# Optimization experiments

Measured on AMD Instinct MI355X. Metric: run time of the kernel, lower is better.

Reference implementation:

```python
import jax, jax.numpy as jnp
import numpy as np

RADIUS = 0.05  # ball-query radius (original default 0.015 is too sparse for unit-cube density)


def setup_inputs() -> dict:
    key = jax.random.key(0)
    k1, k2, k3 = jax.random.split(key, 3)
    B, N_IN, N_OUT = 8, 16384, 8192
    x = jax.random.normal(k1, (B, N_IN), dtype=jnp.float32)
    inp_positions = jax.random.uniform(k2, (N_IN, 3), dtype=jnp.float32)
    out_positions = jax.random.uniform(k3, (N_OUT, 3), dtype=jnp.float32)
    return {"x": x, "inp_positions": inp_positions, "out_positions": out_positions}


def reference(x, inp_positions, out_positions):
    # Radius neighbor mean pooling: for each output point, average x over all
    # input points within RADIUS. Equivalent to the two spmm calls (sum and
    # count) followed by safe division in the original module.
    r2 = RADIUS * RADIUS
    # pairwise squared distances [n_out, n_in]
    d2 = jnp.sum((out_positions[:, None, :] - inp_positions[None, :, :]) ** 2, axis=-1)
    mask = (d2 <= r2).astype(x.dtype)          # sparse adjacency, dense-masked
    counts = jnp.sum(mask, axis=1)             # [n_out] = dem before clamping
    num = jnp.einsum("oi,bi->bo", mask, x)    # [B, n_out]
    dem = jnp.where(counts > 0, counts, jnp.ones_like(counts))
    return num / dem[None, :]
```

## Files before the change

### kernel.cpp

```cpp
#include <hip/hip_runtime.h>

#define TPB   256
#define BINT  64
#define MAXB  8
#define GD    20
#define NC    (GD * GD * GD)
#define CAP   16

static inline int cdiv(int a, int b) { return (a + b - 1) / b; }

#define DPP_ADD_I(x, ctrl, rmask)                                             \
    ((x) + __builtin_amdgcn_update_dpp(0, (x), (ctrl), (rmask), 0xf, true))
#define DPP_ADD_F(x, ctrl, rmask)                                             \
    ((x) + __int_as_float(__builtin_amdgcn_update_dpp(                        \
               0, __float_as_int(x), (ctrl), (rmask), 0xf, true)))

__device__ __forceinline__ int wave_incl_scan_i(int x) {
    x = DPP_ADD_I(x, 0x111, 0xf);
    x = DPP_ADD_I(x, 0x112, 0xf);
    x = DPP_ADD_I(x, 0x114, 0xf);
    x = DPP_ADD_I(x, 0x118, 0xf);
    x = DPP_ADD_I(x, 0x142, 0xa);
    x = DPP_ADD_I(x, 0x143, 0xc);
    return x;
}

template <int CTRL, int RMASK>
__device__ __forceinline__ int dpp_max_step(int x) {
    const int y = __builtin_amdgcn_update_dpp(0, x, CTRL, RMASK, 0xf, true);
    return ((unsigned)x > (unsigned)y) ? x : y;
}
__device__ __forceinline__ int wave_incl_maxscan_u(int x) {
    x = dpp_max_step<0x111, 0xf>(x);
    x = dpp_max_step<0x112, 0xf>(x);
    x = dpp_max_step<0x114, 0xf>(x);
    x = dpp_max_step<0x118, 0xf>(x);
    x = dpp_max_step<0x142, 0xa>(x);
    x = dpp_max_step<0x143, 0xc>(x);
    return x;
}

__device__ __forceinline__ float wave_sum_f(float x) {
    x = DPP_ADD_F(x, 0x111, 0xf);
    x = DPP_ADD_F(x, 0x112, 0xf);
    x = DPP_ADD_F(x, 0x114, 0xf);
    x = DPP_ADD_F(x, 0x118, 0xf);
    x = DPP_ADD_F(x, 0x142, 0xa);
    x = DPP_ADD_F(x, 0x143, 0xc);
    return __int_as_float(__builtin_amdgcn_readlane(__float_as_int(x), 63));
}

__global__ void __launch_bounds__(BINT) bin_kernel(
    const float* __restrict__ x, const float* __restrict__ ip,
    int* __restrict__ counts, float4* __restrict__ bins,
    float* __restrict__ xT, int B, int n_in)
{
    const int i = blockIdx.x * BINT + (int)threadIdx.x;
    if (i >= n_in) return;
    const float px = ip[3 * i], py = ip[3 * i + 1], pz = ip[3 * i + 2];
    const int cx = min(GD - 1, max(0, (int)(px * (float)GD)));
    const int cy = min(GD - 1, max(0, (int)(py * (float)GD)));
    const int cz = min(GD - 1, max(0, (int)(pz * (float)GD)));
    const int cell = (cx * GD + cy) * GD + cz;
    const int slot = atomicAdd(counts + cell, 1);
    if (slot < CAP)
        bins[(size_t)cell * CAP + slot] = make_float4(px, py, pz, __int_as_float(i));
    float v[MAXB];
#pragma unroll
    for (int b = 0; b < MAXB; ++b)
        v[b] = (b < B) ? x[(size_t)b * n_in + i] : 0.0f;
    float4* dst = (float4*)(xT + (size_t)i * MAXB);
    dst[0] = make_float4(v[0], v[1], v[2], v[3]);
    dst[1] = make_float4(v[4], v[5], v[6], v[7]);
}

__global__ void __launch_bounds__(TPB) query_kernel(
    const int* __restrict__ counts, const float4* __restrict__ bins,
    const float* __restrict__ xT, const float* __restrict__ out_pos,
    float* __restrict__ out, int B, int n_out, float r2)
{
    __shared__ int Msh[TPB / 64][64];

    const int lane = (int)threadIdx.x & 63;
    const int wid  = (int)threadIdx.x >> 6;
    const int o    = blockIdx.x * 4 + wid;
    if (o >= n_out) return;

    volatile int* M = &Msh[wid][0];

    const float ox = out_pos[3 * o];
    const float oy = out_pos[3 * o + 1];
    const float oz = out_pos[3 * o + 2];

    const float m = 0.05f + 1e-4f;
    const int cxlo = max(0, (int)floorf((ox - m) * (float)GD));
    const int cxhi = min(GD - 1, (int)floorf((ox + m) * (float)GD));
    const int cylo = max(0, (int)floorf((oy - m) * (float)GD));
    const int cyhi = min(GD - 1, (int)floorf((oy + m) * (float)GD));
    const int czlo = max(0, (int)floorf((oz - m) * (float)GD));
    const int czhi = min(GD - 1, (int)floorf((oz + m) * (float)GD));
    const int nx = cxhi - cxlo + 1, ny = cyhi - cylo + 1, nz = czhi - czlo + 1;
    const int ncell = nx * ny * nz;

    int cnt = 0, cellid = 0;
    if (lane < ncell) {
        int t = lane;
        const int dz = t % nz; t /= nz;
        const int dy = t % ny; t /= ny;
        const int dx = t;
        cellid = ((cxlo + dx) * GD + (cylo + dy)) * GD + (czlo + dz);
        cnt = min(counts[cellid], CAP);
    }

    const int incl = wave_incl_scan_i(cnt);
    const int T    = __builtin_amdgcn_readlane(incl, 63);
    const int excl = incl - cnt;
    const int pack = (excl << 13) | cellid;
    const bool pusher = (lane < ncell) && (cnt > 0);

    float csum = 0.0f;
    float acc[MAXB];
#pragma unroll
    for (int b = 0; b < MAXB; ++b) acc[b] = 0.0f;

    int seed = 0;
    for (int base = 0; base < T; base += 64) {
        const int t = base + lane;
        const bool act = t < T;

        M[lane] = 0;
        __builtin_amdgcn_wave_barrier();
        if (pusher && (unsigned)(excl - base) < 64u)
            M[excl - base] = pack;
        __builtin_amdgcn_wave_barrier();
        int r = M[lane];
        if (lane == 0) r = ((unsigned)r > (unsigned)seed) ? r : seed;
        const int own = wave_incl_maxscan_u(r);
        seed = __builtin_amdgcn_readlane(own, 63);

        const int ej = (unsigned)own >> 13;
        const int cj = own & 0x1FFF;
        float4 cand = make_float4(1e9f, 1e9f, 1e9f, 0.0f);
        if (act) cand = bins[(size_t)cj * CAP + (t - ej)];
        const float dx = ox - cand.x;
        const float dy = oy - cand.y;
        const float dz = oz - cand.z;
        const float d2 = dx * dx + dy * dy + dz * dz;
        if (d2 <= r2) {
            csum += 1.0f;
            const int idx = __float_as_int(cand.w);
            const float4* xv = (const float4*)(xT + (size_t)idx * MAXB);
            const float4 a = xv[0], b4 = xv[1];
            acc[0] += a.x;  acc[1] += a.y;  acc[2] += a.z;  acc[3] += a.w;
            acc[4] += b4.x; acc[5] += b4.y; acc[6] += b4.z; acc[7] += b4.w;
        }
    }

    const float tc = wave_sum_f(csum);
    const float t0 = wave_sum_f(acc[0]);
    const float t1 = wave_sum_f(acc[1]);
    const float t2 = wave_sum_f(acc[2]);
    const float t3 = wave_sum_f(acc[3]);
    const float t4 = wave_sum_f(acc[4]);
    const float t5 = wave_sum_f(acc[5]);
    const float t6 = wave_sum_f(acc[6]);
    const float t7 = wave_sum_f(acc[7]);

    const float cc = (tc > 0.0f) ? tc : 1.0f;
    float v = t0;
    v = (lane == 1) ? t1 : v;
    v = (lane == 2) ? t2 : v;
    v = (lane == 3) ? t3 : v;
    v = (lane == 4) ? t4 : v;
    v = (lane == 5) ? t5 : v;
    v = (lane == 6) ? t6 : v;
    v = (lane == 7) ? t7 : v;
    if (lane < B) out[(size_t)lane * n_out + o] = v / cc;
}

__global__ void __launch_bounds__(TPB) brute_kernel(
    const float* __restrict__ x, const float* __restrict__ ip,
    const float* __restrict__ op, float* __restrict__ out,
    int B, int n_in, int n_out, float r2)
{
    const int o = blockIdx.x * TPB + (int)threadIdx.x;
    if (o >= n_out) return;
    const float ox = op[3 * o], oy = op[3 * o + 1], oz = op[3 * o + 2];
    float cnt = 0.0f, acc[MAXB];
#pragma unroll
    for (int b = 0; b < MAXB; ++b) acc[b] = 0.0f;
    for (int i = 0; i < n_in; ++i) {
        const float dx = ox - ip[3 * i];
        const float dy = oy - ip[3 * i + 1];
        const float dz = oz - ip[3 * i + 2];
        const float d2 = dx * dx + dy * dy + dz * dz;
        if (d2 <= r2) {
            cnt += 1.0f;
            for (int b = 0; b < B && b < MAXB; ++b) acc[b] += x[(size_t)b * n_in + i];
        }
    }
    const float cc = (cnt > 0.0f) ? cnt : 1.0f;
    for (int b = 0; b < B && b < MAXB; ++b)
        out[(size_t)b * n_out + o] = acc[b] / cc;
}

extern "C" void kernel_launch(void* const* d_in, const int* in_sizes, int n_in_args,
                              void* d_out, int out_size, void* d_ws, size_t ws_size,
                              hipStream_t stream) {
    const float* x  = (const float*)d_in[0];
    const float* ip = (const float*)d_in[1];
    const float* op = (const float*)d_in[2];
    float* out = (float*)d_out;

    const int n_in  = in_sizes[1] / 3;
    const int n_out = in_sizes[2] / 3;
    const int B     = in_sizes[0] / n_in;
    const float r2  = (float)(0.05 * 0.05);

    const size_t counts_b = (size_t)NC * sizeof(int);
    const size_t bins_b   = (size_t)NC * CAP * sizeof(float4);
    const size_t xT_b     = (size_t)n_in * MAXB * sizeof(float);
    const size_t need     = counts_b + bins_b + xT_b;

    if (B <= MAXB && ws_size >= need) {
        int*    counts = (int*)d_ws;
        float4* bins   = (float4*)((char*)d_ws + counts_b);
        float*  xT     = (float*)((char*)d_ws + counts_b + bins_b);

        (void)hipMemsetAsync(counts, 0, counts_b, stream);
        bin_kernel<<<cdiv(n_in, BINT), BINT, 0, stream>>>(x, ip, counts, bins, xT,
                                                          B, n_in);
        query_kernel<<<cdiv(n_out, 4), TPB, 0, stream>>>(counts, bins, xT, op, out,
                                                         B, n_out, r2);
    } else {
        brute_kernel<<<cdiv(n_out, TPB), TPB, 0, stream>>>(x, ip, op, out,
                                                           B, n_in, n_out, r2);
    }
}
```

Baseline: 66.79 us.

## Fuse binning and query into one persistent kernel with a grid barrier

Merges the binning kernel and the query kernel into a single persistent launch of 1024 blocks. An atomic-counter grid barrier separates the binning phase from the query phase, and output points are processed in a grid-stride loop over waves. This removes a kernel launch and its inter-kernel gap. In exchange, the kernel depends on all blocks being co-resident, and the spin loop's bail-out could let a block proceed before binning finishes.

```diff
diff --git a/kernel.cpp b/kernel.cpp
--- a/kernel.cpp
+++ b/kernel.cpp
@@ -1,7 +1,7 @@
 #include <hip/hip_runtime.h>
 
 #define TPB   256
-#define BINT  64
+#define GRID  1024
 #define MAXB  8
 #define GD    20
 #define NC    (GD * GD * GD)
@@ -50,132 +50,148 @@
     return __int_as_float(__builtin_amdgcn_readlane(__float_as_int(x), 63));
 }
 
-__global__ void __launch_bounds__(BINT) bin_kernel(
+__global__ void __launch_bounds__(TPB, 4) fused_kernel(
     const float* __restrict__ x, const float* __restrict__ ip,
-    int* __restrict__ counts, float4* __restrict__ bins,
-    float* __restrict__ xT, int B, int n_in)
-{
-    const int i = blockIdx.x * BINT + (int)threadIdx.x;
-    if (i >= n_in) return;
-    const float px = ip[3 * i], py = ip[3 * i + 1], pz = ip[3 * i + 2];
-    const int cx = min(GD - 1, max(0, (int)(px * (float)GD)));
-    const int cy = min(GD - 1, max(0, (int)(py * (float)GD)));
-    const int cz = min(GD - 1, max(0, (int)(pz * (float)GD)));
-    const int cell = (cx * GD + cy) * GD + cz;
-    const int slot = atomicAdd(counts + cell, 1);
-    if (slot < CAP)
-        bins[(size_t)cell * CAP + slot] = make_float4(px, py, pz, __int_as_float(i));
-    float v[MAXB];
-#pragma unroll
-    for (int b = 0; b < MAXB; ++b)
-        v[b] = (b < B) ? x[(size_t)b * n_in + i] : 0.0f;
-    float4* dst = (float4*)(xT + (size_t)i * MAXB);
-    dst[0] = make_float4(v[0], v[1], v[2], v[3]);
-    dst[1] = make_float4(v[4], v[5], v[6], v[7]);
-}
-
-__global__ void __launch_bounds__(TPB) query_kernel(
-    const int* __restrict__ counts, const float4* __restrict__ bins,
-    const float* __restrict__ xT, const float* __restrict__ out_pos,
-    float* __restrict__ out, int B, int n_out, float r2)
+    const float* __restrict__ op,
+    int* __restrict__ counts, int* __restrict__ bar,
+    float4* __restrict__ bins, float* __restrict__ xT,
+    float* __restrict__ out, int B, int n_in, int n_out, float r2)
 {
     __shared__ int Msh[TPB / 64][64];
 
+    const int tid = (int)(blockIdx.x * TPB + threadIdx.x);
+
+    if (tid < n_in) {
+        const int i = tid;
+        const float px = ip[3 * i], py = ip[3 * i + 1], pz = ip[3 * i + 2];
+        const int cx = min(GD - 1, max(0, (int)(px * (float)GD)));
+        const int cy = min(GD - 1, max(0, (int)(py * (float)GD)));
+        const int cz = min(GD - 1, max(0, (int)(pz * (float)GD)));
+        const int cell = (cx * GD + cy) * GD + cz;
+        const int slot = atomicAdd(counts + cell, 1);
+        if (slot < CAP)
+            bins[(size_t)cell * CAP + slot] =
+                make_float4(px, py, pz, __int_as_float(i));
+        float v[MAXB];
+#pragma unroll
+        for (int b = 0; b < MAXB; ++b)
+            v[b] = (b < B) ? x[(size_t)b * n_in + i] : 0.0f;
+        float4* dst = (float4*)(xT + (size_t)i * MAXB);
+        dst[0] = make_float4(v[0], v[1], v[2], v[3]);
+        dst[1] = make_float4(v[4], v[5], v[6], v[7]);
+    }
+
+    __threadfence();
+    __syncthreads();
+    if (threadIdx.x == 0) {
+        atomicAdd(bar, 1);
+        int spins = 0;
+        while (__hip_atomic_load(bar, __ATOMIC_RELAXED,
+                                 __HIP_MEMORY_SCOPE_AGENT) < GRID) {
+            __builtin_amdgcn_s_sleep(8);
+            if (++spins > (1 << 20)) break;
+        }
+    }
+    __syncthreads();
+    __threadfence();
+
     const int lane = (int)threadIdx.x & 63;
     const int wid  = (int)threadIdx.x >> 6;
-    const int o    = blockIdx.x * 4 + wid;
-    if (o >= n_out) return;
-
+    const int wv   = tid >> 6;
+    const int nwv  = (GRID * TPB) >> 6;
     volatile int* M = &Msh[wid][0];
 
-    const float ox = out_pos[3 * o];
-    const float oy = out_pos[3 * o + 1];
-    const float oz = out_pos[3 * o + 2];
-
-    const float m = 0.05f + 1e-4f;
-    const int cxlo = max(0, (int)floorf((ox - m) * (float)GD));
-    const int cxhi = min(GD - 1, (int)floorf((ox + m) * (float)GD));
-    const int cylo = max(0, (int)floorf((oy - m) * (float)GD));
-    const int cyhi = min(GD - 1, (int)floorf((oy + m) * (float)GD));
-    const int czlo = max(0, (int)floorf((oz - m) * (float)GD));
-    const int czhi = min(GD - 1, (int)floorf((oz + m) * (float)GD));
-    const int nx = cxhi - cxlo + 1, ny = cyhi - cylo + 1, nz = czhi - czlo + 1;
-    const int ncell = nx * ny * nz;
-
-    int cnt = 0, cellid = 0;
-    if (lane < ncell) {
-        int t = lane;
-        const int dz = t % nz; t /= nz;
-        const int dy = t % ny; t /= ny;
-        const int dx = t;
-        cellid = ((cxlo + dx) * GD + (cylo + dy)) * GD + (czlo + dz);
-        cnt = min(counts[cellid], CAP);
-    }
-
-    const int incl = wave_incl_scan_i(cnt);
-    const int T    = __builtin_amdgcn_readlane(incl, 63);
-    const int excl = incl - cnt;
-    const int pack = (excl << 13) | cellid;
-    const bool pusher = (lane < ncell) && (cnt > 0);
-
-    float csum = 0.0f;
-    float acc[MAXB];
+    for (int o = wv; o < n_out; o += nwv) {
+        const float ox = op[3 * o];
+        const float oy = op[3 * o + 1];
+        const float oz = op[3 * o + 2];
+
+        const float m = 0.05f + 1e-4f;
+        const int cxlo = max(0, (int)floorf((ox - m) * (float)GD));
+        const int cxhi = min(GD - 1, (int)floorf((ox + m) * (float)GD));
+        const int cylo = max(0, (int)floorf((oy - m) * (float)GD));
+        const int cyhi = min(GD - 1, (int)floorf((oy + m) * (float)GD));
+        const int czlo = max(0, (int)floorf((oz - m) * (float)GD));
+        const int czhi = min(GD - 1, (int)floorf((oz + m) * (float)GD));
+        const int nx = cxhi - cxlo + 1, ny = cylo <= cyhi ? cyhi - cylo + 1 : 0,
+                  nz = czhi - czlo + 1;
+        const int ncell = nx * ny * nz;
+
+        int cnt = 0, cellid = 0;
+        if (lane < ncell) {
+            int t = lane;
+            const int dz = t % nz; t /= nz;
+            const int dy = t % ny; t /= ny;
+            const int dx = t;
+            cellid = ((cxlo + dx) * GD + (cylo + dy)) * GD + (czlo + dz);
+            cnt = min(counts[cellid], CAP);
+        }
+
+        const int incl = wave_incl_scan_i(cnt);
+        const int T    = __builtin_amdgcn_readlane(incl, 63);
+        const int excl = incl - cnt;
+        const int pack = (excl << 13) | cellid;
+        const bool pusher = (lane < ncell) && (cnt > 0);
+
+        float csum = 0.0f;
+        float acc[MAXB];
 #pragma unroll
-    for (int b = 0; b < MAXB; ++b) acc[b] = 0.0f;
-
-    int seed = 0;
-    for (int base = 0; base < T; base += 64) {
-        const int t = base + lane;
-        const bool act = t < T;
-
-        M[lane] = 0;
-        __builtin_amdgcn_wave_barrier();
-        if (pusher && (unsigned)(excl - base) < 64u)
-            M[excl - base] = pack;
-        __builtin_amdgcn_wave_barrier();
-        int r = M[lane];
-        if (lane == 0) r = ((unsigned)r > (unsigned)seed) ? r : seed;
-        const int own = wave_incl_maxscan_u(r);
-        seed = __builtin_amdgcn_readlane(own, 63);
-
-        const int ej = (unsigned)own >> 13;
-        const int cj = own & 0x1FFF;
-        float4 cand = make_float4(1e9f, 1e9f, 1e9f, 0.0f);
-        if (act) cand = bins[(size_t)cj * CAP + (t - ej)];
-        const float dx = ox - cand.x;
-        const float dy = oy - cand.y;
-        const float dz = oz - cand.z;
-        const float d2 = dx * dx + dy * dy + dz * dz;
-        if (d2 <= r2) {
-            csum += 1.0f;
-            const int idx = __float_as_int(cand.w);
-            const float4* xv = (const float4*)(xT + (size_t)idx * MAXB);
-            const float4 a = xv[0], b4 = xv[1];
-            acc[0] += a.x;  acc[1] += a.y;  acc[2] += a.z;  acc[3] += a.w;
-            acc[4] += b4.x; acc[5] += b4.y; acc[6] += b4.z; acc[7] += b4.w;
-        }
-    }
-
-    const float tc = wave_sum_f(csum);
-    const float t0 = wave_sum_f(acc[0]);
-    const float t1 = wave_sum_f(acc[1]);
-    const float t2 = wave_sum_f(acc[2]);
-    const float t3 = wave_sum_f(acc[3]);
-    const float t4 = wave_sum_f(acc[4]);
-    const float t5 = wave_sum_f(acc[5]);
-    const float t6 = wave_sum_f(acc[6]);
-    const float t7 = wave_sum_f(acc[7]);
-
-    const float cc = (tc > 0.0f) ? tc : 1.0f;
-    float v = t0;
-    v = (lane == 1) ? t1 : v;
-    v = (lane == 2) ? t2 : v;
-    v = (lane == 3) ? t3 : v;
-    v = (lane == 4) ? t4 : v;
-    v = (lane == 5) ? t5 : v;
-    v = (lane == 6) ? t6 : v;
-    v = (lane == 7) ? t7 : v;
-    if (lane < B) out[(size_t)lane * n_out + o] = v / cc;
+        for (int b = 0; b < MAXB; ++b) acc[b] = 0.0f;
+
+        int seed = 0;
+        for (int base = 0; base < T; base += 64) {
+            const int t = base + lane;
+            const bool act = t < T;
+
+            M[lane] = 0;
+            __builtin_amdgcn_wave_barrier();
+            if (pusher && (unsigned)(excl - base) < 64u)
+                M[excl - base] = pack;
+            __builtin_amdgcn_wave_barrier();
+            int r = M[lane];
+            if (lane == 0) r = ((unsigned)r > (unsigned)seed) ? r : seed;
+            const int own = wave_incl_maxscan_u(r);
+            seed = __builtin_amdgcn_readlane(own, 63);
+
+            const int ej = (unsigned)own >> 13;
+            const int cj = own & 0x1FFF;
+            float4 cand = make_float4(1e9f, 1e9f, 1e9f, 0.0f);
+            if (act) cand = bins[(size_t)cj * CAP + (t - ej)];
+            const float dx = ox - cand.x;
+            const float dy = oy - cand.y;
+            const float dz = oz - cand.z;
+            const float d2 = dx * dx + dy * dy + dz * dz;
+            if (d2 <= r2) {
+                csum += 1.0f;
+                const int idx = __float_as_int(cand.w);
+                const float4* xv = (const float4*)(xT + (size_t)idx * MAXB);
+                const float4 a = xv[0], b4 = xv[1];
+                acc[0] += a.x;  acc[1] += a.y;  acc[2] += a.z;  acc[3] += a.w;
+                acc[4] += b4.x; acc[5] += b4.y; acc[6] += b4.z; acc[7] += b4.w;
+            }
+        }
+
+        const float tc = wave_sum_f(csum);
+        const float t0 = wave_sum_f(acc[0]);
+        const float t1 = wave_sum_f(acc[1]);
+        const float t2 = wave_sum_f(acc[2]);
+        const float t3 = wave_sum_f(acc[3]);
+        const float t4 = wave_sum_f(acc[4]);
+        const float t5 = wave_sum_f(acc[5]);
+        const float t6 = wave_sum_f(acc[6]);
+        const float t7 = wave_sum_f(acc[7]);
+
+        const float cc = (tc > 0.0f) ? tc : 1.0f;
+        float v = t0;
+        v = (lane == 1) ? t1 : v;
+        v = (lane == 2) ? t2 : v;
+        v = (lane == 3) ? t3 : v;
+        v = (lane == 4) ? t4 : v;
+        v = (lane == 5) ? t5 : v;
+        v = (lane == 6) ? t6 : v;
+        v = (lane == 7) ? t7 : v;
+        if (lane < B) out[(size_t)lane * n_out + o] = v / cc;
+    }
 }
 
 __global__ void __launch_bounds__(TPB) brute_kernel(
@@ -217,21 +233,21 @@
     const int B     = in_sizes[0] / n_in;
     const float r2  = (float)(0.05 * 0.05);
 
-    const size_t counts_b = (size_t)NC * sizeof(int);
-    const size_t bins_b   = (size_t)NC * CAP * sizeof(float4);
-    const size_t xT_b     = (size_t)n_in * MAXB * sizeof(float);
-    const size_t need     = counts_b + bins_b + xT_b;
-
-    if (B <= MAXB && ws_size >= need) {
+    const size_t zero_b  = 32768;
+    const size_t bins_b  = (size_t)NC * CAP * sizeof(float4);
+    const size_t xT_b    = (size_t)n_in * MAXB * sizeof(float);
+    const size_t need    = zero_b + bins_b + xT_b;
+
+    if (B <= MAXB && ws_size >= need && n_in <= GRID * TPB) {
         int*    counts = (int*)d_ws;
-        float4* bins   = (float4*)((char*)d_ws + counts_b);
-        float*  xT     = (float*)((char*)d_ws + counts_b + bins_b);
-
-        (void)hipMemsetAsync(counts, 0, counts_b, stream);
-        bin_kernel<<<cdiv(n_in, BINT), BINT, 0, stream>>>(x, ip, counts, bins, xT,
-                                                          B, n_in);
-        query_kernel<<<cdiv(n_out, 4), TPB, 0, stream>>>(counts, bins, xT, op, out,
-                                                         B, n_out, r2);
+        int*    bar    = (int*)((char*)d_ws + (size_t)NC * sizeof(int));
+        float4* bins   = (float4*)((char*)d_ws + zero_b);
+        float*  xT     = (float*)((char*)d_ws + zero_b + bins_b);
+
+        (void)hipMemsetAsync(d_ws, 0, zero_b, stream);
+        fused_kernel<<<GRID, TPB, 0, stream>>>(x, ip, op, counts, bar,
+                                               bins, xT, out,
+                                               B, n_in, n_out, r2);
     } else {
         brute_kernel<<<cdiv(n_out, TPB), TPB, 0, stream>>>(x, ip, op, out,
                                                            B, n_in, n_out, r2);
```

Result: slower. 235.7 us (+252.9%).

## Bin points per cell slice in LDS and drop the counts memset

Applied to the files above, without the earlier changes.

Replaces the global-atomic binning kernel with one where each of 256 blocks owns a 32-cell slice. Every block scans all input positions and bins only the points that fall in its slice, using LDS atomics, then writes counts and bins out with coalesced stores. The transpose of x is split across the same blocks. This removes the hipMemsetAsync launch and the global atomics, but every block now rereads the whole position array, and bin slot order within a cell changes.

```diff
diff --git a/kernel.cpp b/kernel.cpp
--- a/kernel.cpp
+++ b/kernel.cpp
@@ -1,11 +1,12 @@
 #include <hip/hip_runtime.h>
 
-#define TPB   256
-#define BINT  64
-#define MAXB  8
-#define GD    20
-#define NC    (GD * GD * GD)
-#define CAP   16
+#define TPB    256
+#define BIN2G  256
+#define SLICE  32
+#define MAXB   8
+#define GD     20
+#define NC     (GD * GD * GD)
+#define CAP    16
 
 static inline int cdiv(int a, int b) { return (a + b - 1) / b; }
 
@@ -50,28 +51,57 @@
     return __int_as_float(__builtin_amdgcn_readlane(__float_as_int(x), 63));
 }
 
-__global__ void __launch_bounds__(BINT) bin_kernel(
+__global__ void __launch_bounds__(TPB) bin2_kernel(
     const float* __restrict__ x, const float* __restrict__ ip,
     int* __restrict__ counts, float4* __restrict__ bins,
     float* __restrict__ xT, int B, int n_in)
 {
-    const int i = blockIdx.x * BINT + (int)threadIdx.x;
-    if (i >= n_in) return;
-    const float px = ip[3 * i], py = ip[3 * i + 1], pz = ip[3 * i + 2];
-    const int cx = min(GD - 1, max(0, (int)(px * (float)GD)));
-    const int cy = min(GD - 1, max(0, (int)(py * (float)GD)));
-    const int cz = min(GD - 1, max(0, (int)(pz * (float)GD)));
-    const int cell = (cx * GD + cy) * GD + cz;
-    const int slot = atomicAdd(counts + cell, 1);
-    if (slot < CAP)
-        bins[(size_t)cell * CAP + slot] = make_float4(px, py, pz, __int_as_float(i));
-    float v[MAXB];
+    __shared__ int    cnt_lds[SLICE];
+    __shared__ float4 bin_lds[SLICE][CAP];
+
+    const int tid = (int)threadIdx.x;
+    const int blk = (int)blockIdx.x;
+    const int lo  = blk * SLICE;
+
+    if (tid < SLICE) cnt_lds[tid] = 0;
+    for (int s = tid; s < SLICE * CAP; s += TPB)
+        ((float4*)bin_lds)[s] = make_float4(0.f, 0.f, 0.f, 0.f);
+    __syncthreads();
+
+    for (int i = tid; i < n_in; i += TPB) {
+        const float px = ip[3 * i], py = ip[3 * i + 1], pz = ip[3 * i + 2];
+        const int cx = min(GD - 1, max(0, (int)(px * (float)GD)));
+        const int cy = min(GD - 1, max(0, (int)(py * (float)GD)));
+        const int cz = min(GD - 1, max(0, (int)(pz * (float)GD)));
+        const int cell = (cx * GD + cy) * GD + cz;
+        const int rel  = cell - lo;
+        if ((unsigned)rel < (unsigned)SLICE) {
+            const int slot = atomicAdd(&cnt_lds[rel], 1);
+            if (slot < CAP)
+                bin_lds[rel][slot] = make_float4(px, py, pz, __int_as_float(i));
+        }
+    }
+    __syncthreads();
+
+    const int ncells = min(NC - lo, SLICE);
+    if (ncells > 0) {
+        if (tid < ncells) counts[lo + tid] = cnt_lds[tid];
+        for (int s = tid; s < ncells * CAP; s += TPB)
+            bins[(size_t)lo * CAP + s] = ((float4*)bin_lds)[s];
+    }
+
+    const int per = (n_in + BIN2G - 1) / BIN2G;
+    const int i0  = blk * per;
+    const int ie  = min(i0 + per, n_in);
+    for (int i = i0 + tid; i < ie; i += TPB) {
+        float v[MAXB];
 #pragma unroll
-    for (int b = 0; b < MAXB; ++b)
-        v[b] = (b < B) ? x[(size_t)b * n_in + i] : 0.0f;
-    float4* dst = (float4*)(xT + (size_t)i * MAXB);
-    dst[0] = make_float4(v[0], v[1], v[2], v[3]);
-    dst[1] = make_float4(v[4], v[5], v[6], v[7]);
+        for (int b = 0; b < MAXB; ++b)
+            v[b] = (b < B) ? x[(size_t)b * n_in + i] : 0.0f;
+        float4* dst = (float4*)(xT + (size_t)i * MAXB);
+        dst[0] = make_float4(v[0], v[1], v[2], v[3]);
+        dst[1] = make_float4(v[4], v[5], v[6], v[7]);
+    }
 }
 
 __global__ void __launch_bounds__(TPB) query_kernel(
@@ -217,7 +247,7 @@
     const int B     = in_sizes[0] / n_in;
     const float r2  = (float)(0.05 * 0.05);
 
-    const size_t counts_b = (size_t)NC * sizeof(int);
+    const size_t counts_b = 32768;
     const size_t bins_b   = (size_t)NC * CAP * sizeof(float4);
     const size_t xT_b     = (size_t)n_in * MAXB * sizeof(float);
     const size_t need     = counts_b + bins_b + xT_b;
@@ -227,9 +257,7 @@
         float4* bins   = (float4*)((char*)d_ws + counts_b);
         float*  xT     = (float*)((char*)d_ws + counts_b + bins_b);
 
-        (void)hipMemsetAsync(counts, 0, counts_b, stream);
-        bin_kernel<<<cdiv(n_in, BINT), BINT, 0, stream>>>(x, ip, counts, bins, xT,
-                                                          B, n_in);
+        bin2_kernel<<<BIN2G, TPB, 0, stream>>>(x, ip, counts, bins, xT, B, n_in);
         query_kernel<<<cdiv(n_out, 4), TPB, 0, stream>>>(counts, bins, xT, op, out,
                                                          B, n_out, r2);
     } else {
```

Result: slower. 85.36 us (+27.8%).

## Replace counts memset with generation-tagged cell counters in global device memory

Applied to the files above, without the earlier changes.

Drops the per-call hipMemsetAsync on the cell counts. Counters now live in a persistent device global and carry a generation tag in their high bits. bin_kernel uses a CAS loop that resets a counter lazily when its tag is stale, and the last query block to finish bumps the generation for the next call. This removes one launch and its gaps, but turns the atomicAdd into a CAS retry loop under contention. It also depends on cross-kernel global state, and g_gen_q is written by one bin block and read with no explicit fence.

```diff
diff --git a/kernel.cpp b/kernel.cpp
--- a/kernel.cpp
+++ b/kernel.cpp
@@ -8,6 +8,11 @@
 #define CAP   16
 
 static inline int cdiv(int a, int b) { return (a + b - 1) / b; }
+
+__device__ unsigned g_counts[NC];
+__device__ unsigned g_gen   = 1u;
+__device__ unsigned g_gen_q = 0u;
+__device__ unsigned g_done  = 0u;
 
 #define DPP_ADD_I(x, ctrl, rmask)                                             \
     ((x) + __builtin_amdgcn_update_dpp(0, (x), (ctrl), (rmask), 0xf, true))
@@ -52,9 +57,11 @@
 
 __global__ void __launch_bounds__(BINT) bin_kernel(
     const float* __restrict__ x, const float* __restrict__ ip,
-    int* __restrict__ counts, float4* __restrict__ bins,
-    float* __restrict__ xT, int B, int n_in)
+    float4* __restrict__ bins, float* __restrict__ xT, int B, int n_in)
 {
+    const unsigned gen = g_gen & 0xFFFFFFu;
+    if (blockIdx.x == 0 && threadIdx.x == 0) g_gen_q = gen;
+
     const int i = blockIdx.x * BINT + (int)threadIdx.x;
     if (i >= n_in) return;
     const float px = ip[3 * i], py = ip[3 * i + 1], pz = ip[3 * i + 2];
@@ -62,9 +69,25 @@
     const int cy = min(GD - 1, max(0, (int)(py * (float)GD)));
     const int cz = min(GD - 1, max(0, (int)(pz * (float)GD)));
     const int cell = (cx * GD + cy) * GD + cz;
-    const int slot = atomicAdd(counts + cell, 1);
+
+    int slot;
+    unsigned expected = g_counts[cell];
+    while (true) {
+        unsigned newval;
+        if ((expected >> 8) == gen) {
+            slot = (int)(expected & 0xFFu);
+            newval = (slot >= 0xFF) ? expected : expected + 1u;
+        } else {
+            slot = 0;
+            newval = (gen << 8) | 1u;
+        }
+        const unsigned prev = atomicCAS(&g_counts[cell], expected, newval);
+        if (prev == expected) break;
+        expected = prev;
+    }
     if (slot < CAP)
         bins[(size_t)cell * CAP + slot] = make_float4(px, py, pz, __int_as_float(i));
+
     float v[MAXB];
 #pragma unroll
     for (int b = 0; b < MAXB; ++b)
@@ -75,107 +98,119 @@
 }
 
 __global__ void __launch_bounds__(TPB) query_kernel(
-    const int* __restrict__ counts, const float4* __restrict__ bins,
-    const float* __restrict__ xT, const float* __restrict__ out_pos,
-    float* __restrict__ out, int B, int n_out, float r2)
+    const float4* __restrict__ bins, const float* __restrict__ xT,
+    const float* __restrict__ out_pos, float* __restrict__ out,
+    int B, int n_out, float r2)
 {
     __shared__ int Msh[TPB / 64][64];
 
+    const unsigned gen = g_gen_q;
     const int lane = (int)threadIdx.x & 63;
     const int wid  = (int)threadIdx.x >> 6;
     const int o    = blockIdx.x * 4 + wid;
-    if (o >= n_out) return;
-
-    volatile int* M = &Msh[wid][0];
-
-    const float ox = out_pos[3 * o];
-    const float oy = out_pos[3 * o + 1];
-    const float oz = out_pos[3 * o + 2];
-
-    const float m = 0.05f + 1e-4f;
-    const int cxlo = max(0, (int)floorf((ox - m) * (float)GD));
-    const int cxhi = min(GD - 1, (int)floorf((ox + m) * (float)GD));
-    const int cylo = max(0, (int)floorf((oy - m) * (float)GD));
-    const int cyhi = min(GD - 1, (int)floorf((oy + m) * (float)GD));
-    const int czlo = max(0, (int)floorf((oz - m) * (float)GD));
-    const int czhi = min(GD - 1, (int)floorf((oz + m) * (float)GD));
-    const int nx = cxhi - cxlo + 1, ny = cyhi - cylo + 1, nz = czhi - czlo + 1;
-    const int ncell = nx * ny * nz;
-
-    int cnt = 0, cellid = 0;
-    if (lane < ncell) {
-        int t = lane;
-        const int dz = t % nz; t /= nz;
-        const int dy = t % ny; t /= ny;
-        const int dx = t;
-        cellid = ((cxlo + dx) * GD + (cylo + dy)) * GD + (czlo + dz);
-        cnt = min(counts[cellid], CAP);
-    }
-
-    const int incl = wave_incl_scan_i(cnt);
-    const int T    = __builtin_amdgcn_readlane(incl, 63);
-    const int excl = incl - cnt;
-    const int pack = (excl << 13) | cellid;
-    const bool pusher = (lane < ncell) && (cnt > 0);
-
-    float csum = 0.0f;
-    float acc[MAXB];
+
+    if (o < n_out) {
+        volatile int* M = &Msh[wid][0];
+
+        const float ox = out_pos[3 * o];
+        const float oy = out_pos[3 * o + 1];
+        const float oz = out_pos[3 * o + 2];
+
+        const float m = 0.05f + 1e-4f;
+        const int cxlo = max(0, (int)floorf((ox - m) * (float)GD));
+        const int cxhi = min(GD - 1, (int)floorf((ox + m) * (float)GD));
+        const int cylo = max(0, (int)floorf((oy - m) * (float)GD));
+        const int cyhi = min(GD - 1, (int)floorf((oy + m) * (float)GD));
+        const int czlo = max(0, (int)floorf((oz - m) * (float)GD));
+        const int czhi = min(GD - 1, (int)floorf((oz + m) * (float)GD));
+        const int nx = cxhi - cxlo + 1, ny = cyhi - cylo + 1, nz = czhi - czlo + 1;
+        const int ncell = nx * ny * nz;
+
+        int cnt = 0, cellid = 0;
+        if (lane < ncell) {
+            int t = lane;
+            const int dz = t % nz; t /= nz;
+            const int dy = t % ny; t /= ny;
+            const int dx = t;
+            cellid = ((cxlo + dx) * GD + (cylo + dy)) * GD + (czlo + dz);
+            const unsigned raw = g_counts[cellid];
+            cnt = ((raw >> 8) == gen) ? min((int)(raw & 0xFFu), CAP) : 0;
+        }
+
+        const int incl = wave_incl_scan_i(cnt);
+        const int T    = __builtin_amdgcn_readlane(incl, 63);
+        const int excl = incl - cnt;
+        const int pack = (excl << 13) | cellid;
+        const bool pusher = (lane < ncell) && (cnt > 0);
+
+        float csum = 0.0f;
+        float acc[MAXB];
 #pragma unroll
-    for (int b = 0; b < MAXB; ++b) acc[b] = 0.0f;
-
-    int seed = 0;
-    for (int base = 0; base < T; base += 64) {
-        const int t = base + lane;
-        const bool act = t < T;
-
-        M[lane] = 0;
-        __builtin_amdgcn_wave_barrier();
-        if (pusher && (unsigned)(excl - base) < 64u)
-            M[excl - base] = pack;
-        __builtin_amdgcn_wave_barrier();
-        int r = M[lane];
-        if (lane == 0) r = ((unsigned)r > (unsigned)seed) ? r : seed;
-        const int own = wave_incl_maxscan_u(r);
-        seed = __builtin_amdgcn_readlane(own, 63);
-
-        const int ej = (unsigned)own >> 13;
-        const int cj = own & 0x1FFF;
-        float4 cand = make_float4(1e9f, 1e9f, 1e9f, 0.0f);
-        if (act) cand = bins[(size_t)cj * CAP + (t - ej)];
-        const float dx = ox - cand.x;
-        const float dy = oy - cand.y;
-        const float dz = oz - cand.z;
-        const float d2 = dx * dx + dy * dy + dz * dz;
-        if (d2 <= r2) {
-            csum += 1.0f;
-            const int idx = __float_as_int(cand.w);
-            const float4* xv = (const float4*)(xT + (size_t)idx * MAXB);
-            const float4 a = xv[0], b4 = xv[1];
-            acc[0] += a.x;  acc[1] += a.y;  acc[2] += a.z;  acc[3] += a.w;
-            acc[4] += b4.x; acc[5] += b4.y; acc[6] += b4.z; acc[7] += b4.w;
-        }
-    }
-
-    const float tc = wave_sum_f(csum);
-    const float t0 = wave_sum_f(acc[0]);
-    const float t1 = wave_sum_f(acc[1]);
-    const float t2 = wave_sum_f(acc[2]);
-    const float t3 = wave_sum_f(acc[3]);
-    const float t4 = wave_sum_f(acc[4]);
-    const float t5 = wave_sum_f(acc[5]);
-    const float t6 = wave_sum_f(acc[6]);
-    const float t7 = wave_sum_f(acc[7]);
-
-    const float cc = (tc > 0.0f) ? tc : 1.0f;
-    float v = t0;
-    v = (lane == 1) ? t1 : v;
-    v = (lane == 2) ? t2 : v;
-    v = (lane == 3) ? t3 : v;
-    v = (lane == 4) ? t4 : v;
-    v = (lane == 5) ? t5 : v;
-    v = (lane == 6) ? t6 : v;
-    v = (lane == 7) ? t7 : v;
-    if (lane < B) out[(size_t)lane * n_out + o] = v / cc;
+        for (int b = 0; b < MAXB; ++b) acc[b] = 0.0f;
+
+        int seed = 0;
+        for (int base = 0; base < T; base += 64) {
+            const int t = base + lane;
+            const bool act = t < T;
+
+            M[lane] = 0;
+            __builtin_amdgcn_wave_barrier();
+            if (pusher && (unsigned)(excl - base) < 64u)
+                M[excl - base] = pack;
+            __builtin_amdgcn_wave_barrier();
+            int r = M[lane];
+            if (lane == 0) r = ((unsigned)r > (unsigned)seed) ? r : seed;
+            const int own = wave_incl_maxscan_u(r);
+            seed = __builtin_amdgcn_readlane(own, 63);
+
+            const int ej = (unsigned)own >> 13;
+            const int cj = own & 0x1FFF;
+            float4 cand = make_float4(1e9f, 1e9f, 1e9f, 0.0f);
+            if (act) cand = bins[(size_t)cj * CAP + (t - ej)];
+            const float dx = ox - cand.x;
+            const float dy = oy - cand.y;
+            const float dz = oz - cand.z;
+            const float d2 = dx * dx + dy * dy + dz * dz;
+            if (d2 <= r2) {
+                csum += 1.0f;
+                const int idx = __float_as_int(cand.w);
+                const float4* xv = (const float4*)(xT + (size_t)idx * MAXB);
+                const float4 a = xv[0], b4 = xv[1];
+                acc[0] += a.x;  acc[1] += a.y;  acc[2] += a.z;  acc[3] += a.w;
+                acc[4] += b4.x; acc[5] += b4.y; acc[6] += b4.z; acc[7] += b4.w;
+            }
+        }
+
+        const float tc = wave_sum_f(csum);
+        const float t0 = wave_sum_f(acc[0]);
+        const float t1 = wave_sum_f(acc[1]);
+        const float t2 = wave_sum_f(acc[2]);
+        const float t3 = wave_sum_f(acc[3]);
+        const float t4 = wave_sum_f(acc[4]);
+        const float t5 = wave_sum_f(acc[5]);
+        const float t6 = wave_sum_f(acc[6]);
+        const float t7 = wave_sum_f(acc[7]);
+
+        const float cc = (tc > 0.0f) ? tc : 1.0f;
+        float v = t0;
+        v = (lane == 1) ? t1 : v;
+        v = (lane == 2) ? t2 : v;
+        v = (lane == 3) ? t3 : v;
+        v = (lane == 4) ? t4 : v;
+        v = (lane == 5) ? t5 : v;
+        v = (lane == 6) ? t6 : v;
+        v = (lane == 7) ? t7 : v;
+        if (lane < B) out[(size_t)lane * n_out + o] = v / cc;
+    }
+
+    __syncthreads();
+    if (threadIdx.x == 0) {
+        const unsigned old = atomicAdd(&g_done, 1u);
+        if (old == (unsigned)gridDim.x - 1u) {
+            g_done = 0u;
+            g_gen  = gen + 1u;
+        }
+    }
 }
 
 __global__ void __launch_bounds__(TPB) brute_kernel(
@@ -217,20 +252,16 @@
     const int B     = in_sizes[0] / n_in;
     const float r2  = (float)(0.05 * 0.05);
 
-    const size_t counts_b = (size_t)NC * sizeof(int);
-    const size_t bins_b   = (size_t)NC * CAP * sizeof(float4);
-    const size_t xT_b     = (size_t)n_in * MAXB * sizeof(float);
-    const size_t need     = counts_b + bins_b + xT_b;
+    const size_t bins_b = (size_t)NC * CAP * sizeof(float4);
+    const size_t xT_b   = (size_t)n_in * MAXB * sizeof(float);
+    const size_t need   = bins_b + xT_b;
 
     if (B <= MAXB && ws_size >= need) {
-        int*    counts = (int*)d_ws;
-        float4* bins   = (float4*)((char*)d_ws + counts_b);
-        float*  xT     = (float*)((char*)d_ws + counts_b + bins_b);
-
-        (void)hipMemsetAsync(counts, 0, counts_b, stream);
-        bin_kernel<<<cdiv(n_in, BINT), BINT, 0, stream>>>(x, ip, counts, bins, xT,
-                                                          B, n_in);
-        query_kernel<<<cdiv(n_out, 4), TPB, 0, stream>>>(counts, bins, xT, op, out,
+        float4* bins = (float4*)d_ws;
+        float*  xT   = (float*)((char*)d_ws + bins_b);
+
+        bin_kernel<<<cdiv(n_in, BINT), BINT, 0, stream>>>(x, ip, bins, xT, B, n_in);
+        query_kernel<<<cdiv(n_out, 4), TPB, 0, stream>>>(bins, xT, op, out,
                                                          B, n_out, r2);
     } else {
         brute_kernel<<<cdiv(n_out, TPB), TPB, 0, stream>>>(x, ip, op, out,
```

Result: slower. 91.88 us (+37.5%).
